# Kernel optimization log

Measured on AMD Instinct MI355X. Metric: run time of the kernel, lower is better.

Reference implementation:

```python
import jax, jax.numpy as jnp
import numpy as np

NUM_HEADS = 8
EMBED_DIM = 128
HEAD_DIM = EMBED_DIM // NUM_HEADS  # 16
NB_FEATURES = EMBED_DIM            # 128
EPS = 1e-4


def _make_projection(nb_rows, nb_cols, rng):
    # gaussian_orthogonal_random_matrix with scaling=0
    blocks = []
    for _ in range(nb_rows // nb_cols):
        q, _ = np.linalg.qr(rng.standard_normal((nb_cols, nb_cols)))
        blocks.append(q.T)
    rem = nb_rows - (nb_rows // nb_cols) * nb_cols
    if rem > 0:
        q, _ = np.linalg.qr(rng.standard_normal((nb_cols, nb_cols)))
        blocks.append(q.T[:rem])
    final = np.concatenate(blocks, axis=0)
    mult = np.linalg.norm(rng.standard_normal((nb_rows, nb_cols)), axis=1)
    return (mult[:, None] * final).astype(np.float32)


def setup_inputs() -> dict:
    key = jax.random.key(0)
    ks = jax.random.split(key, 7)
    R, C, E = 8, 2048, EMBED_DIM
    s = 1.0 / np.sqrt(E)
    x = jax.random.normal(ks[0], (R, C, E), dtype=jnp.float32)
    Wq = jax.random.uniform(ks[1], (E, E), jnp.float32, -s, s)
    bq = jax.random.uniform(ks[2], (E,), jnp.float32, -s, s)
    Wk = jax.random.uniform(ks[3], (E, E), jnp.float32, -s, s)
    bk = jax.random.uniform(ks[4], (E,), jnp.float32, -s, s)
    Wv = jax.random.uniform(ks[5], (E, E), jnp.float32, -s, s)
    bv = jax.random.uniform(ks[6], (E,), jnp.float32, -s, s)
    proj = jnp.asarray(_make_projection(NB_FEATURES, HEAD_DIM, np.random.default_rng(0)))
    return {"x": x, "Wq": Wq, "bq": bq, "Wk": Wk, "bk": bk, "Wv": Wv, "bv": bv, "proj": proj}


def _softmax_kernel(data, proj, is_query):
    # data: (R, h, n, d); proj: (F, d)
    d = data.shape[-1]
    normalizer = d ** (-0.25)
    ratio = proj.shape[0] ** (-0.5)
    data_dash = jnp.einsum('rhnd,jd->rhnj', normalizer * data, proj)  # (R,h,n,F)
    diag = jnp.sum(data * data, axis=-1, keepdims=True) * 0.5 * normalizer ** 2
    if is_query:
        m = jnp.max(data_dash, axis=-1, keepdims=True)
    else:
        m = jnp.max(data_dash, axis=(-1, -2), keepdims=True)
    return ratio * (jnp.exp(data_dash - diag - m) + EPS)


def reference(x, Wq, bq, Wk, bk, Wv, bv, proj):
    R, C, E = x.shape
    h, hd = NUM_HEADS, HEAD_DIM

    def proj_heads(W, b):
        y = jnp.einsum('rce,fe->rcf', x, W) + b
        return y.reshape(R, C, h, hd).transpose(0, 2, 1, 3)  # (R,h,C,hd)

    q = _softmax_kernel(proj_heads(Wq, bq), proj, is_query=True)   # (R,h,C,F)
    k = _softmax_kernel(proj_heads(Wk, bk), proj, is_query=False)  # (R,h,C,F)
    v = proj_heads(Wv, bv)                                          # (R,h,C,hd)

    # fold batch (R) into the feature dim: (h, C, R*F) / (h, C, R*hd)
    qf = q.transpose(1, 2, 0, 3).reshape(h, C, R * NB_FEATURES)
    kf = k.transpose(1, 2, 0, 3).reshape(h, C, R * NB_FEATURES)
    vf = v.transpose(1, 2, 0, 3).reshape(h, C, R * hd)

    k_sum = kf.sum(axis=-2)                                   # (h, D)
    D_inv = 1.0 / jnp.einsum('hnd,hd->hn', qf, k_sum)         # (h, C)
    context = jnp.einsum('hnd,hne->hde', kf, vf)              # (h, D, Ev)
    out = jnp.einsum('hde,hnd,hn->hne', context, qf, D_inv)   # (h, C, R*hd)

    out = out.reshape(h, C, R, hd).transpose(2, 1, 0, 3).reshape(R, C, E)
    attn = jnp.einsum('hqf,hkf->hqk', qf, kf)                 # (h, C, C)
    return out, attn
```

## Files before the change

kernel.cpp:

```cpp
#include <hip/hip_runtime.h>
#include <hip/hip_bf16.h>
#include <stdint.h>

typedef __bf16 bf16x8 __attribute__((ext_vector_type(8)));
typedef __bf16 bf16x4 __attribute__((ext_vector_type(4)));
typedef float  f32x4  __attribute__((ext_vector_type(4)));

#define RATIO 0.08838834764831845f
#define EPSV  1e-4f

#define GLOBAL_AS __attribute__((address_space(1)))
#define LDS_AS    __attribute__((address_space(3)))

static __device__ __forceinline__ void gload16(const void* g, void* l) {
  __builtin_amdgcn_global_load_lds((GLOBAL_AS const void*)g, (LDS_AS void*)l, 16, 0, 0);
}

static constexpr size_t OFF_XB    = 0;
static constexpr size_t OFF_WCAT  = OFF_XB    + 4194304;
static constexpr size_t OFF_MQ    = OFF_WCAT  + 98304;
static constexpr size_t OFF_MK    = OFF_MQ    + 262144;
static constexpr size_t OFF_BCAT  = OFF_MK    + 262144;
static constexpr size_t OFF_BQF   = OFF_BCAT  + 2048;
static constexpr size_t OFF_BKF   = OFF_BQF   + 4096;
static constexpr size_t OFF_Y     = OFF_BKF   + 4096;
static constexpr size_t OFF_QF    = OFF_Y     + 25165824;
static constexpr size_t OFF_KF    = OFF_QF    + 33554432;
static constexpr size_t OFF_KFT   = OFF_KF    + 33554432;
static constexpr size_t OFF_VFT   = OFF_KFT   + 33554432;
static constexpr size_t OFF_KPART = OFF_VFT   + 4194304;
static constexpr size_t OFF_KMAX  = OFF_KPART + 4096;
static constexpr size_t OFF_KSPART= OFF_KMAX  + 1024;
static constexpr size_t OFF_DPART = OFF_KSPART+ 524288;
static constexpr size_t OFF_CTXP  = OFF_DPART + 524288;
static constexpr size_t OFF_CTXT  = OFF_CTXP  + 16777216;
static constexpr size_t WS_NEED   = OFF_CTXT  + 2097152;

static __device__ __forceinline__ void gemm_core(
    const __hip_bfloat16* __restrict__ A, const __hip_bfloat16* __restrict__ B,
    int lda, int ldb, int K, int tm, int tn,
    __bf16* As, __bf16* Bs, f32x4 acc[4][4]) {
  const int t    = threadIdx.x;
  const int w    = t >> 6;
  const int lane = t & 63;
  const int m_off = (w >> 1) << 6;
  const int n_off = (w & 1) << 6;
  const int r0 = t >> 2;
  const int kk = (t & 3) << 3;
  char* Asb = (char*)As + (w << 10);
  char* Bsb = (char*)Bs + (w << 10);
  const int frow = lane & 15;
  const int koff = (lane >> 4) << 3;
  for (int k0 = 0; k0 < K; k0 += 32) {
    const __hip_bfloat16* Ag = A + (size_t)(tm + r0) * lda + (k0 + kk);
    const __hip_bfloat16* Bg = B + (size_t)(tn + r0) * ldb + (k0 + kk);
    gload16(Ag, Asb);
    gload16(Ag + (size_t)64 * lda, Asb + 4096);
    gload16(Bg, Bsb);
    gload16(Bg + (size_t)64 * ldb, Bsb + 4096);
    __syncthreads();
    bf16x8 af[4], bfr[4];
#pragma unroll
    for (int mi = 0; mi < 4; ++mi)
      af[mi] = *(const bf16x8*)(As + ((m_off + mi * 16 + frow) << 5) + koff);
#pragma unroll
    for (int ni = 0; ni < 4; ++ni)
      bfr[ni] = *(const bf16x8*)(Bs + ((n_off + ni * 16 + frow) << 5) + koff);
#pragma unroll
    for (int mi = 0; mi < 4; ++mi)
#pragma unroll
      for (int ni = 0; ni < 4; ++ni)
        acc[mi][ni] = __builtin_amdgcn_mfma_f32_16x16x32_bf16(af[mi], bfr[ni], acc[mi][ni], 0, 0, 0);
    __syncthreads();
  }
}

static __device__ __forceinline__ void gemm_core_k128(
    const __hip_bfloat16* __restrict__ A, const __hip_bfloat16* __restrict__ B,
    int lda, int ldb, int tm, int tn,
    __bf16* As, __bf16* Bs, f32x4 acc[4][4]) {
  const int t = threadIdx.x, w = t >> 6, lane = t & 63;
  const int m_off = (w >> 1) << 6, n_off = (w & 1) << 6;
  const int frow = lane & 15;
  const int g0 = lane >> 4;
  const int srow = (w << 5) + (lane >> 4);
  const int sg = lane & 15;
  char* Ab = (char*)As + (w << 13);
  char* Bb = (char*)Bs + (w << 13);
#pragma unroll
  for (int j = 0; j < 8; ++j) {
    const int row = srow + (j << 2);
    const int scol = (sg ^ (row & 15)) << 3;
    gload16(A + (size_t)(tm + row) * lda + scol, Ab + (j << 10));
    gload16(B + (size_t)(tn + row) * ldb + scol, Bb + (j << 10));
  }
  __syncthreads();
#pragma unroll
  for (int kk = 0; kk < 4; ++kk) {
    bf16x8 af[4], bfr[4];
#pragma unroll
    for (int mi = 0; mi < 4; ++mi) {
      const int row = m_off + mi * 16 + frow;
      const int gr = ((kk << 2) + g0) ^ (row & 15);
      af[mi] = *(const bf16x8*)((char*)As + row * 256 + gr * 16);
    }
#pragma unroll
    for (int ni = 0; ni < 4; ++ni) {
      const int row = n_off + ni * 16 + frow;
      const int gr = ((kk << 2) + g0) ^ (row & 15);
      bfr[ni] = *(const bf16x8*)((char*)Bs + row * 256 + gr * 16);
    }
#pragma unroll
    for (int mi = 0; mi < 4; ++mi)
#pragma unroll
      for (int ni = 0; ni < 4; ++ni)
        acc[mi][ni] = __builtin_amdgcn_mfma_f32_16x16x32_bf16(af[mi], bfr[ni], acc[mi][ni], 0, 0, 0);
  }
  __syncthreads();
}

#define ZERO_ACC(acc) do {                                   \
  _Pragma("unroll") for (int a_ = 0; a_ < 4; ++a_)           \
  _Pragma("unroll") for (int b_ = 0; b_ < 4; ++b_)           \
    acc[a_][b_] = (f32x4){0.f, 0.f, 0.f, 0.f};               \
} while (0)

__global__ void k_prep(const float* __restrict__ x,
                       const float* __restrict__ Wq, const float* __restrict__ bq,
                       const float* __restrict__ Wk, const float* __restrict__ bk,
                       const float* __restrict__ Wv, const float* __restrict__ bv,
                       const float* __restrict__ proj,
                       __hip_bfloat16* __restrict__ xb,
                       __hip_bfloat16* __restrict__ Wcat, float* __restrict__ bcat,
                       __hip_bfloat16* __restrict__ Mq, __hip_bfloat16* __restrict__ Mk,
                       float* __restrict__ bqf, float* __restrict__ bkf) {
  const int b = blockIdx.x, t = threadIdx.x;
  {
    int i = (b * 256 + t) * 4;
    f32x4 v = *(const f32x4*)(x + i);
#pragma unroll
    for (int j = 0; j < 4; ++j) xb[i + j] = __float2bfloat16(v[j]);
  }
  if (b < 1024) {
    int i = b * 256 + t;
    {
      int which = i >> 17;
      int rem = i & 131071;
      int hj = rem >> 7, e = rem & 127;
      int hh = hj >> 7, j = hj & 127;
      const float* W = which ? Wk : Wq;
      float s = 0.f;
#pragma unroll
      for (int u = 0; u < 16; ++u) s += proj[j * 16 + u] * W[(hh * 16 + u) * 128 + e];
      if (which) Mk[rem] = __float2bfloat16(0.5f * s);
      else       Mq[rem] = __float2bfloat16(0.5f * s);
    }
    if (i < 2048) {
      int which = i >> 10;
      int hj = i & 1023, hh = hj >> 7, j = hj & 127;
      const float* bb = which ? bk : bq;
      float s = 0.f;
#pragma unroll
      for (int u = 0; u < 16; ++u) s += proj[j * 16 + u] * bb[hh * 16 + u];
      if (which) bkf[hj] = 0.5f * s;
      else       bqf[hj] = 0.5f * s;
    }
  }
  if (b < 192) {
    int i = b * 256 + t;
    int mat = i >> 14, rem = i & 16383;
    const float* W = (mat == 0) ? Wq : ((mat == 1) ? Wk : Wv);
    Wcat[i] = __float2bfloat16(W[rem]);
    if (i < 384) {
      int m2 = i >> 7;
      const float* bb = (m2 == 0) ? bq : ((m2 == 1) ? bk : bv);
      bcat[i] = bb[i & 127];
    }
  }
}

__global__ __launch_bounds__(256) void k_proj(
    const __hip_bfloat16* __restrict__ xb, const __hip_bfloat16* __restrict__ Wcat,
    const float* __restrict__ bcat, float* __restrict__ Y,
    __hip_bfloat16* __restrict__ vfT) {
  __shared__ __align__(16) char pool[65536];
  __bf16* As = (__bf16*)pool;
  __bf16* Bs = (__bf16*)(pool + 32768);
  const int tm = blockIdx.x << 7, tn = blockIdx.y << 7;
  f32x4 acc[4][4];
  ZERO_ACC(acc);
  gemm_core_k128(xb, Wcat, 128, 128, tm, tn, As, Bs, acc);
  const int t = threadIdx.x, w = t >> 6, lane = t & 63;
  const int m_off = (w >> 1) << 6, n_off = (w & 1) << 6;
  const int frow = lane & 15;
  if (tn == 256) {
    __bf16* vT = (__bf16*)pool;
#pragma unroll
    for (int ni = 0; ni < 4; ++ni) {
      const int j = n_off + ni * 16 + frow;
      const float bias = bcat[256 + j];
#pragma unroll
      for (int mi = 0; mi < 4; ++mi)
#pragma unroll
        for (int i = 0; i < 4; ++i) {
          const int rl = m_off + mi * 16 + ((lane >> 4) << 2) + i;
          vT[j * 136 + rl] = (__bf16)(acc[mi][ni][i] + bias);
        }
    }
    __syncthreads();
    const int r = tm >> 11, c0 = tm & 2047;
    const int j2 = t >> 1, half = t & 1;
    const int hh = j2 >> 4, aa = j2 & 15;
    __bf16* dst = (__bf16*)vfT + (((size_t)(hh * 128 + r * 16 + aa)) << 11) + c0 + (half << 6);
    const __bf16* srcr = vT + j2 * 136 + (half << 6);
#pragma unroll
    for (int q8 = 0; q8 < 8; ++q8)
      *(bf16x8*)(dst + (q8 << 3)) = *(const bf16x8*)(srcr + (q8 << 3));
  } else {
#pragma unroll
    for (int ni = 0; ni < 4; ++ni) {
      const int col = tn + n_off + ni * 16 + frow;
      const float bias = bcat[col];
#pragma unroll
      for (int mi = 0; mi < 4; ++mi)
#pragma unroll
        for (int i = 0; i < 4; ++i) {
          const int row = tm + m_off + mi * 16 + ((lane >> 4) << 2) + i;
          Y[(size_t)row * 384 + col] = acc[mi][ni][i] + bias;
        }
    }
  }
}

__global__ __launch_bounds__(256) void k_dashk_max(
    const __hip_bfloat16* __restrict__ xb, const __hip_bfloat16* __restrict__ Mk,
    const float* __restrict__ bkf, float* __restrict__ kpart) {
  __shared__ __align__(16) char pool[65536];
  __shared__ float wmax[4];
  __bf16* As = (__bf16*)pool;
  __bf16* Bs = (__bf16*)(pool + 32768);
  const int h = blockIdx.y;
  const int tm = blockIdx.x << 7;
  f32x4 acc[4][4];
  ZERO_ACC(acc);
  gemm_core_k128(xb, Mk + h * 16384, 128, 128, tm, 0, As, Bs, acc);
  const int t = threadIdx.x, w = t >> 6, lane = t & 63;
  const int n_off = (w & 1) << 6;
  float mx = -1e30f;
#pragma unroll
  for (int ni = 0; ni < 4; ++ni) {
    const float bia = bkf[h * 128 + n_off + ni * 16 + (lane & 15)];
#pragma unroll
    for (int mi = 0; mi < 4; ++mi)
#pragma unroll
      for (int i = 0; i < 4; ++i) mx = fmaxf(mx, acc[mi][ni][i] + bia);
  }
#pragma unroll
  for (int off = 1; off < 64; off <<= 1) mx = fmaxf(mx, __shfl_xor(mx, off));
  if (lane == 0) wmax[w] = mx;
  __syncthreads();
  if (t == 0) kpart[h * 128 + blockIdx.x] = fmaxf(fmaxf(wmax[0], wmax[1]), fmaxf(wmax[2], wmax[3]));
}

__global__ __launch_bounds__(256) void k_dashk_feat(
    const __hip_bfloat16* __restrict__ xb, const __hip_bfloat16* __restrict__ Mk,
    const float* __restrict__ bkf, const float* __restrict__ Y,
    const float* __restrict__ kpart,
    __hip_bfloat16* __restrict__ kf, __hip_bfloat16* __restrict__ kfT,
    float* __restrict__ kspart) {
  __shared__ __align__(16) char pool[65536];
  __shared__ float diag_s[128];
  __shared__ float ksp_s[2][128];
  __bf16* As = (__bf16*)pool;
  __bf16* Bs = (__bf16*)(pool + 32768);
  __bf16* kT = (__bf16*)pool;
  const int h = blockIdx.y;
  const int tm = blockIdx.x << 7;
  const int t = threadIdx.x, w = t >> 6, lane = t & 63;
  if (t < 128) {
    const float* yp = Y + (size_t)(tm + t) * 384 + 128 + h * 16;
    float s = 0.f;
#pragma unroll
    for (int u = 0; u < 16; ++u) s += yp[u] * yp[u];
    diag_s[t] = 0.125f * s;
  }
  f32x4 acc[4][4];
  ZERO_ACC(acc);
  gemm_core_k128(xb, Mk + h * 16384, 128, 128, tm, 0, As, Bs, acc);
  const int m_off = (w >> 1) << 6, n_off = (w & 1) << 6;
  const int frow = lane & 15;
  const int r = tm >> 11;
  const int c0 = tm & 2047;
  const int cb = blockIdx.x & 15;
  float m = -1e30f;
  {
    const float* kp = kpart + h * 128 + r * 16;
#pragma unroll
    for (int i = 0; i < 16; ++i) m = fmaxf(m, kp[i]);
  }
  float bia[4];
#pragma unroll
  for (int ni = 0; ni < 4; ++ni) bia[ni] = bkf[h * 128 + n_off + ni * 16 + frow];
  float ksp[4] = {0.f, 0.f, 0.f, 0.f};
#pragma unroll
  for (int mi = 0; mi < 4; ++mi) {
#pragma unroll
    for (int i = 0; i < 4; ++i) {
      const int rl = m_off + mi * 16 + ((lane >> 4) << 2) + i;
      const int c = c0 + rl;
      const float dm = diag_s[rl] + m;
#pragma unroll
      for (int ni = 0; ni < 4; ++ni) {
        const int j = n_off + ni * 16 + frow;
        const float f = RATIO * (__expf(acc[mi][ni][i] + bia[ni] - dm) + EPSV);
        const __hip_bfloat16 hb = __float2bfloat16(f);
        kf[((size_t)((h << 11) + c) << 10) + (r << 7) + j] = hb;
        kT[j * 136 + rl] = (__bf16)f;
        ksp[ni] += __bfloat162float(hb);
      }
    }
  }
#pragma unroll
  for (int ni = 0; ni < 4; ++ni) {
    ksp[ni] += __shfl_xor(ksp[ni], 16);
    ksp[ni] += __shfl_xor(ksp[ni], 32);
  }
  if ((lane >> 4) == 0) {
#pragma unroll
    for (int ni = 0; ni < 4; ++ni)
      ksp_s[w >> 1][n_off + ni * 16 + frow] = ksp[ni];
  }
  __syncthreads();
  if (t < 128)
    kspart[(((cb << 3) + h) << 10) + r * 128 + t] = ksp_s[0][t] + ksp_s[1][t];
  const int j2 = t >> 1, half = t & 1;
  __bf16* dst = (__bf16*)kfT + (((size_t)(h << 10) + (r << 7) + j2) << 11) + c0 + (half << 6);
  const __bf16* srcr = kT + j2 * 136 + (half << 6);
#pragma unroll
  for (int q8 = 0; q8 < 8; ++q8)
    *(bf16x8*)(dst + (q8 << 3)) = *(const bf16x8*)(srcr + (q8 << 3));
}

__global__ __launch_bounds__(256) void k_dashq(
    const __hip_bfloat16* __restrict__ xb, const __hip_bfloat16* __restrict__ Mq,
    const float* __restrict__ bqf, const float* __restrict__ Y,
    const float* __restrict__ kspart,
    __hip_bfloat16* __restrict__ qf, float* __restrict__ dpart) {
  __shared__ __align__(16) char pool[65536];
  __shared__ float diag_s[128];
  __shared__ float rmax_s[2][128];
  __shared__ float ksum_s[128];
  __shared__ float dred_s[2][128];
  __bf16* As = (__bf16*)pool;
  __bf16* Bs = (__bf16*)(pool + 32768);
  const int h = blockIdx.y;
  const int tm = blockIdx.x << 7;
  const int r = tm >> 11, c0 = tm & 2047;
  f32x4 acc[4][4];
  ZERO_ACC(acc);
  const int t = threadIdx.x, w = t >> 6, lane = t & 63;
  if (t < 128) {
    const float* yp = Y + (size_t)(tm + t) * 384 + h * 16;
    float s = 0.f;
#pragma unroll
    for (int u = 0; u < 16; ++u) s += yp[u] * yp[u];
    diag_s[t] = 0.125f * s;
    float ks = 0.f;
#pragma unroll
    for (int cb = 0; cb < 16; ++cb) ks += kspart[(((cb << 3) + h) << 10) + r * 128 + t];
    ksum_s[t] = ks;
  }
  gemm_core_k128(xb, Mq + h * 16384, 128, 128, tm, 0, As, Bs, acc);
  const int m_off = (w >> 1) << 6, n_off = (w & 1) << 6;
  const int frow = lane & 15;
  float bia[4];
#pragma unroll
  for (int ni = 0; ni < 4; ++ni) bia[ni] = bqf[h * 128 + n_off + ni * 16 + frow];
  float rmx[4][4];
#pragma unroll
  for (int mi = 0; mi < 4; ++mi)
#pragma unroll
    for (int i = 0; i < 4; ++i) {
      float m0 = acc[mi][0][i] + bia[0];
      m0 = fmaxf(m0, acc[mi][1][i] + bia[1]);
      m0 = fmaxf(m0, acc[mi][2][i] + bia[2]);
      m0 = fmaxf(m0, acc[mi][3][i] + bia[3]);
      rmx[mi][i] = m0;
    }
#pragma unroll
  for (int off = 1; off < 16; off <<= 1)
#pragma unroll
    for (int mi = 0; mi < 4; ++mi)
#pragma unroll
      for (int i = 0; i < 4; ++i)
        rmx[mi][i] = fmaxf(rmx[mi][i], __shfl_xor(rmx[mi][i], off));
  if (frow == 0) {
#pragma unroll
    for (int mi = 0; mi < 4; ++mi)
#pragma unroll
      for (int i = 0; i < 4; ++i)
        rmax_s[w & 1][m_off + mi * 16 + ((lane >> 4) << 2) + i] = rmx[mi][i];
  }
  __syncthreads();
  float p[4][4];
#pragma unroll
  for (int mi = 0; mi < 4; ++mi)
#pragma unroll
    for (int i = 0; i < 4; ++i) p[mi][i] = 0.f;
#pragma unroll
  for (int mi = 0; mi < 4; ++mi) {
#pragma unroll
    for (int i = 0; i < 4; ++i) {
      const int rl = m_off + mi * 16 + ((lane >> 4) << 2) + i;
      const float md = diag_s[rl] + fmaxf(rmax_s[0][rl], rmax_s[1][rl]);
#pragma unroll
      for (int ni = 0; ni < 4; ++ni) {
        const int j = n_off + ni * 16 + frow;
        const float f = RATIO * (__expf(acc[mi][ni][i] + bia[ni] - md) + EPSV);
        const __hip_bfloat16 hb = __float2bfloat16(f);
        qf[((size_t)((h << 11) + c0 + rl) << 10) + (r << 7) + j] = hb;
        p[mi][i] += __bfloat162float(hb) * ksum_s[j];
      }
    }
  }
#pragma unroll
  for (int off = 1; off < 16; off <<= 1)
#pragma unroll
    for (int mi = 0; mi < 4; ++mi)
#pragma unroll
      for (int i = 0; i < 4; ++i)
        p[mi][i] += __shfl_xor(p[mi][i], off);
  if (frow == 0) {
#pragma unroll
    for (int mi = 0; mi < 4; ++mi)
#pragma unroll
      for (int i = 0; i < 4; ++i)
        dred_s[w & 1][m_off + mi * 16 + ((lane >> 4) << 2) + i] = p[mi][i];
  }
  __syncthreads();
  if (t < 128)
    dpart[(((r << 3) + h) << 11) + c0 + t] = dred_s[0][t] + dred_s[1][t];
}

#define SBAR() __builtin_amdgcn_s_barrier()
#define FEN()  do { asm volatile("" ::: "memory"); __builtin_amdgcn_sched_barrier(0); } while (0)
#define PRIO1() __builtin_amdgcn_s_setprio(1)
#define PRIO0() __builtin_amdgcn_s_setprio(0)
#define VMW4() do { asm volatile("s_waitcnt vmcnt(4)" ::: "memory"); } while (0)
#define VMW0() do { asm volatile("s_waitcnt vmcnt(0)" ::: "memory"); } while (0)

#define MFMA16(nlo) do {                                                      \
  _Pragma("unroll") for (int mi_ = 0; mi_ < 8; ++mi_)                         \
  _Pragma("unroll") for (int nj_ = 0; nj_ < 2; ++nj_)                         \
    acc[mi_][(nlo) + nj_] = __builtin_amdgcn_mfma_f32_16x16x32_bf16(          \
        aR[mi_], bR[nj_], acc[mi_][(nlo) + nj_], 0, 0, 0);                    \
} while (0)

__global__ __launch_bounds__(512, 2) void k_attn8(
    const __hip_bfloat16* __restrict__ qf, const __hip_bfloat16* __restrict__ kf,
    float* __restrict__ attn) {
  extern __shared__ __align__(128) char lds[];
  const int lid = blockIdx.x;
  const int swz = ((lid & 7) << 6) + (lid >> 3);
  const int h  = swz >> 6;
  const int tm = ((swz >> 3) & 7) << 8;
  const int tn = (swz & 7) << 8;
  const __hip_bfloat16* Ag = qf + ((size_t)h << 21);
  const __hip_bfloat16* Bg = kf + ((size_t)h << 21);

  const int t = threadIdx.x, wid = t >> 6, lane = t & 63;
  const int f = lane & 15;
  const int wr = wid >> 2, wc = wid & 3;
  const int swzg = (((lane >> 4) ^ ((f >> 1) & 3)) << 4);
  const int aoff = ((wr << 7) + f) * 64 + swzg;
  const int boff = 65536 + ((wc << 6) + f) * 64 + swzg;
  const int srow = t >> 2;
  const int scol = (((t & 3) ^ ((t >> 3) & 3)) << 3);
  const int sdst = wid << 10;

  f32x4 acc[8][4] = {};
  bf16x8 aR[8], bR[2];

  auto stageA = [&](int buf, int kh, int k0) {
    char* d = lds + buf * 32768 + kh * 16384 + sdst;
    const __hip_bfloat16* g = Ag + (size_t)(tm + srow) * 1024 + k0 + (kh << 5) + scol;
    gload16(g, d);
    gload16(g + 128 * 1024, d + 8192);
  };
  auto stageB = [&](int buf, int kh, int k0) {
    char* d = lds + 65536 + buf * 32768 + kh * 16384 + sdst;
    const __hip_bfloat16* g = Bg + (size_t)(tn + srow) * 1024 + k0 + (kh << 5) + scol;
    gload16(g, d);
    gload16(g + 128 * 1024, d + 8192);
  };

  stageA(0, 0, 0); stageB(0, 0, 0); stageA(0, 1, 0); stageB(0, 1, 0);
  VMW4();
  SBAR(); FEN();

  for (int kt = 0; kt < 15; ++kt) {
    const int buf = kt & 1, nbuf = buf ^ 1;
    const int bo = buf * 32768;
    const int nk0 = (kt + 1) << 6;
#pragma unroll
    for (int mi = 0; mi < 8; ++mi) aR[mi] = *(const bf16x8*)(lds + bo + aoff + mi * 1024);
    bR[0] = *(const bf16x8*)(lds + bo + boff);
    bR[1] = *(const bf16x8*)(lds + bo + boff + 1024);
    stageA(nbuf, 0, nk0);
    PRIO1(); MFMA16(0); PRIO0();
    bR[0] = *(const bf16x8*)(lds + bo + boff + 2048);
    bR[1] = *(const bf16x8*)(lds + bo + boff + 3072);
    stageB(nbuf, 0, nk0);
    PRIO1(); MFMA16(2); PRIO0();
    VMW4();
    SBAR(); FEN();
#pragma unroll
    for (int mi = 0; mi < 8; ++mi) aR[mi] = *(const bf16x8*)(lds + bo + 16384 + aoff + mi * 1024);
    bR[0] = *(const bf16x8*)(lds + bo + 16384 + boff);
    bR[1] = *(const bf16x8*)(lds + bo + 16384 + boff + 1024);
    stageA(nbuf, 1, nk0);
    PRIO1(); MFMA16(0); PRIO0();
    bR[0] = *(const bf16x8*)(lds + bo + 16384 + boff + 2048);
    bR[1] = *(const bf16x8*)(lds + bo + 16384 + boff + 3072);
    stageB(nbuf, 1, nk0);
    PRIO1(); MFMA16(2); PRIO0();
    VMW4();
    SBAR(); FEN();
  }
  {
    const int bo = 32768;
#pragma unroll
    for (int mi = 0; mi < 8; ++mi) aR[mi] = *(const bf16x8*)(lds + bo + aoff + mi * 1024);
    bR[0] = *(const bf16x8*)(lds + bo + boff);
    bR[1] = *(const bf16x8*)(lds + bo + boff + 1024);
    PRIO1(); MFMA16(0); PRIO0();
    bR[0] = *(const bf16x8*)(lds + bo + boff + 2048);
    bR[1] = *(const bf16x8*)(lds + bo + boff + 3072);
    PRIO1(); MFMA16(2); PRIO0();
    VMW0();
    SBAR(); FEN();
#pragma unroll
    for (int mi = 0; mi < 8; ++mi) aR[mi] = *(const bf16x8*)(lds + bo + 16384 + aoff + mi * 1024);
    bR[0] = *(const bf16x8*)(lds + bo + 16384 + boff);
    bR[1] = *(const bf16x8*)(lds + bo + 16384 + boff + 1024);
    PRIO1(); MFMA16(0); PRIO0();
    bR[0] = *(const bf16x8*)(lds + bo + 16384 + boff + 2048);
    bR[1] = *(const bf16x8*)(lds + bo + 16384 + boff + 3072);
    PRIO1(); MFMA16(2); PRIO0();
  }

  float* Cc = attn + ((size_t)h << 22);
  const int rbase = tm + (wr << 7) + ((lane >> 4) << 2);
  const int cbase = tn + (wc << 6) + f;
#pragma unroll
  for (int mi = 0; mi < 8; ++mi)
#pragma unroll
    for (int i = 0; i < 4; ++i) {
      float* rp = Cc + ((size_t)(rbase + mi * 16 + i) << 11) + cbase;
#pragma unroll
      for (int ni = 0; ni < 4; ++ni) rp[ni * 16] = acc[mi][ni][i];
    }
}

__global__ __launch_bounds__(256) void k_ctx(
    const __hip_bfloat16* __restrict__ vfT, const __hip_bfloat16* __restrict__ kfT,
    float* __restrict__ ctxp) {
  __shared__ __align__(16) __bf16 As[4096], Bs[4096];
  const int z = blockIdx.z, h = z >> 2, kc = z & 3;
  const int tn = blockIdx.y << 7;
  f32x4 acc[4][4];
  ZERO_ACC(acc);
  gemm_core(vfT + ((size_t)h << 18) + (kc << 9), kfT + ((size_t)h << 21) + (kc << 9),
            2048, 2048, 512, 0, tn, As, Bs, acc);
  float* Cp = ctxp + ((size_t)(kc * 8 + h) << 17);
  const int t = threadIdx.x, w = t >> 6, lane = t & 63;
  const int m_off = (w >> 1) << 6, n_off = (w & 1) << 6;
#pragma unroll
  for (int mi = 0; mi < 4; ++mi)
#pragma unroll
    for (int i = 0; i < 4; ++i) {
      const int row = m_off + mi * 16 + ((lane >> 4) << 2) + i;
#pragma unroll
      for (int ni = 0; ni < 4; ++ni) {
        const int col = tn + n_off + ni * 16 + (lane & 15);
        Cp[((size_t)row << 10) + col] = acc[mi][ni][i];
      }
    }
}

__global__ void k_ctxred(const float* __restrict__ ctxp, __hip_bfloat16* __restrict__ ctxT) {
  const int i = (blockIdx.x * 256 + threadIdx.x) * 4;
  f32x4 a = *(const f32x4*)(ctxp + i);
  f32x4 b = *(const f32x4*)(ctxp + i + 1048576);
  f32x4 c = *(const f32x4*)(ctxp + i + 2097152);
  f32x4 d = *(const f32x4*)(ctxp + i + 3145728);
  bf16x4 o;
#pragma unroll
  for (int j = 0; j < 4; ++j) o[j] = (__bf16)(a[j] + b[j] + c[j] + d[j]);
  *(bf16x4*)((__bf16*)ctxT + i) = o;
}

__global__ __launch_bounds__(256) void k_out64(
    const __hip_bfloat16* __restrict__ qf, const __hip_bfloat16* __restrict__ ctxT,
    const float* __restrict__ dpart, float* __restrict__ outp) {
  __shared__ __align__(16) __bf16 As[2048], Bs[4096];
  __shared__ float dinv_s[64];
  const int h = blockIdx.z;
  const int tm = blockIdx.x << 6;
  const int t = threadIdx.x, w = t >> 6, lane = t & 63;
  if (t < 64) {
    float s = 0.f;
#pragma unroll
    for (int r = 0; r < 8; ++r) s += dpart[(((r << 3) + h) << 11) + tm + t];
    dinv_s[t] = 1.0f / s;
  }
  const int m_off = (w >> 1) << 5, n_off = (w & 1) << 6;
  const int r0 = t >> 2, kk = (t & 3) << 3;
  char* Asb = (char*)As + ((t >> 6) << 10);
  char* Bsb = (char*)Bs + ((t >> 6) << 10);
  const int frow = lane & 15, koff = (lane >> 4) << 3;
  const __hip_bfloat16* A = qf + ((size_t)h << 21);
  const __hip_bfloat16* B = ctxT + ((size_t)h << 17);
  f32x4 acc[2][4];
#pragma unroll
  for (int a_ = 0; a_ < 2; ++a_)
#pragma unroll
    for (int b_ = 0; b_ < 4; ++b_) acc[a_][b_] = (f32x4){0.f, 0.f, 0.f, 0.f};
  for (int k0 = 0; k0 < 1024; k0 += 32) {
    const __hip_bfloat16* Agp = A + (size_t)(tm + r0) * 1024 + (k0 + kk);
    const __hip_bfloat16* Bgp = B + (size_t)r0 * 1024 + (k0 + kk);
    gload16(Agp, Asb);
    gload16(Bgp, Bsb);
    gload16(Bgp + (size_t)64 * 1024, Bsb + 4096);
    __syncthreads();
    bf16x8 af[2], bfr[4];
#pragma unroll
    for (int mi = 0; mi < 2; ++mi)
      af[mi] = *(const bf16x8*)(As + ((m_off + mi * 16 + frow) << 5) + koff);
#pragma unroll
    for (int ni = 0; ni < 4; ++ni)
      bfr[ni] = *(const bf16x8*)(Bs + ((n_off + ni * 16 + frow) << 5) + koff);
#pragma unroll
    for (int mi = 0; mi < 2; ++mi)
#pragma unroll
      for (int ni = 0; ni < 4; ++ni)
        acc[mi][ni] = __builtin_amdgcn_mfma_f32_16x16x32_bf16(af[mi], bfr[ni], acc[mi][ni], 0, 0, 0);
    __syncthreads();
  }
#pragma unroll
  for (int mi = 0; mi < 2; ++mi)
#pragma unroll
    for (int i = 0; i < 4; ++i) {
      const int rl = m_off + mi * 16 + ((lane >> 4) << 2) + i;
      const int row = tm + rl;
      const float dv = dinv_s[rl];
#pragma unroll
      for (int ni = 0; ni < 4; ++ni) {
        const int col = n_off + ni * 16 + frow;
        const int rb = col >> 4, tt = col & 15;
        outp[(((size_t)(rb << 11) + row) << 7) + (h << 4) + tt] = acc[mi][ni][i] * dv;
      }
    }
}

extern "C" void kernel_launch(void* const* d_in, const int* in_sizes, int n_in,
                              void* d_out, int out_size, void* d_ws, size_t ws_size,
                              hipStream_t stream) {
  const float* x    = (const float*)d_in[0];
  const float* Wq   = (const float*)d_in[1];
  const float* bq   = (const float*)d_in[2];
  const float* Wk   = (const float*)d_in[3];
  const float* bk   = (const float*)d_in[4];
  const float* Wv   = (const float*)d_in[5];
  const float* bv   = (const float*)d_in[6];
  const float* proj = (const float*)d_in[7];
  if (ws_size < WS_NEED) return;

  char* ws = (char*)d_ws;
  __hip_bfloat16* xb   = (__hip_bfloat16*)(ws + OFF_XB);
  __hip_bfloat16* Wcat = (__hip_bfloat16*)(ws + OFF_WCAT);
  __hip_bfloat16* Mq   = (__hip_bfloat16*)(ws + OFF_MQ);
  __hip_bfloat16* Mk   = (__hip_bfloat16*)(ws + OFF_MK);
  float* bcat = (float*)(ws + OFF_BCAT);
  float* bqf  = (float*)(ws + OFF_BQF);
  float* bkf  = (float*)(ws + OFF_BKF);
  float* Y    = (float*)(ws + OFF_Y);
  __hip_bfloat16* qf  = (__hip_bfloat16*)(ws + OFF_QF);
  __hip_bfloat16* kf  = (__hip_bfloat16*)(ws + OFF_KF);
  __hip_bfloat16* kfT = (__hip_bfloat16*)(ws + OFF_KFT);
  __hip_bfloat16* vfT = (__hip_bfloat16*)(ws + OFF_VFT);
  float* kpart  = (float*)(ws + OFF_KPART);
  float* kspart = (float*)(ws + OFF_KSPART);
  float* dpart  = (float*)(ws + OFF_DPART);
  float* ctxp   = (float*)(ws + OFF_CTXP);
  __hip_bfloat16* ctxT = (__hip_bfloat16*)(ws + OFF_CTXT);

  float* outp = (float*)d_out;
  float* attn = (float*)d_out + 2097152;

  static int attr_done = 0;
  if (!attr_done) {
    (void)hipFuncSetAttribute((const void*)k_attn8,
                              hipFuncAttributeMaxDynamicSharedMemorySize, 131072);
    attr_done = 1;
  }

  k_prep<<<dim3(2048), dim3(256), 0, stream>>>(x, Wq, bq, Wk, bk, Wv, bv, proj,
                                               xb, Wcat, bcat, Mq, Mk, bqf, bkf);
  k_proj<<<dim3(128, 3), dim3(256), 0, stream>>>(xb, Wcat, bcat, Y, vfT);
  k_dashk_max<<<dim3(128, 8), dim3(256), 0, stream>>>(xb, Mk, bkf, kpart);
  k_dashk_feat<<<dim3(128, 8), dim3(256), 0, stream>>>(xb, Mk, bkf, Y, kpart, kf, kfT, kspart);
  k_dashq<<<dim3(128, 8), dim3(256), 0, stream>>>(xb, Mq, bqf, Y, kspart, qf, dpart);
  k_attn8<<<dim3(512), dim3(512), 131072, stream>>>(qf, kf, attn);
  k_ctx<<<dim3(1, 8, 32), dim3(256), 0, stream>>>(vfT, kfT, ctxp);
  k_ctxred<<<dim3(1024), dim3(256), 0, stream>>>(ctxp, ctxT);
  k_out64<<<dim3(32, 1, 8), dim3(256), 0, stream>>>(qf, ctxT, dpart, outp);
}
```

Before: 183.8 us.

## Replace double-buffered attn GEMM loop with a four-stage LDS ring prefetch

The attention GEMM main loop switches from two 64-wide K buffers, each processed in halves, to a four-slot ring of 32-wide K tiles. Loads run three tiles ahead, and each iteration waits with vmcnt(8). Each iteration loads all A and B fragments up front and issues 32 MFMAs in one block instead of two groups of 16. The goal is to hide global-to-LDS latency with a deeper prefetch while keeping total LDS use the same. The risk is extra registers for the four B fragments and a fixed barrier per 32-K step.

```diff
diff --git a/kernel.cpp b/kernel.cpp
--- a/kernel.cpp
+++ b/kernel.cpp
@@ -446,14 +446,15 @@
 #define FEN()  do { asm volatile("" ::: "memory"); __builtin_amdgcn_sched_barrier(0); } while (0)
 #define PRIO1() __builtin_amdgcn_s_setprio(1)
 #define PRIO0() __builtin_amdgcn_s_setprio(0)
+#define VMW8() do { asm volatile("s_waitcnt vmcnt(8)" ::: "memory"); } while (0)
 #define VMW4() do { asm volatile("s_waitcnt vmcnt(4)" ::: "memory"); } while (0)
 #define VMW0() do { asm volatile("s_waitcnt vmcnt(0)" ::: "memory"); } while (0)
 
-#define MFMA16(nlo) do {                                                      \
+#define MFMA32() do {                                                         \
   _Pragma("unroll") for (int mi_ = 0; mi_ < 8; ++mi_)                         \
-  _Pragma("unroll") for (int nj_ = 0; nj_ < 2; ++nj_)                         \
-    acc[mi_][(nlo) + nj_] = __builtin_amdgcn_mfma_f32_16x16x32_bf16(          \
-        aR[mi_], bR[nj_], acc[mi_][(nlo) + nj_], 0, 0, 0);                    \
+  _Pragma("unroll") for (int nj_ = 0; nj_ < 4; ++nj_)                         \
+    acc[mi_][nj_] = __builtin_amdgcn_mfma_f32_16x16x32_bf16(                  \
+        aR[mi_], bR[nj_], acc[mi_][nj_], 0, 0, 0);                            \
 } while (0)
 
 __global__ __launch_bounds__(512, 2) void k_attn8(
@@ -471,82 +472,52 @@
   const int t = threadIdx.x, wid = t >> 6, lane = t & 63;
   const int f = lane & 15;
   const int wr = wid >> 2, wc = wid & 3;
-  const int swzg = (((lane >> 4) ^ ((f >> 1) & 3)) << 4);
-  const int aoff = ((wr << 7) + f) * 64 + swzg;
-  const int boff = 65536 + ((wc << 6) + f) * 64 + swzg;
+  const int swzg = (((lane >> 4) ^ ((lane >> 1) & 3)) << 4);
+  const int abase = ((wr << 7) + f) * 64 + swzg;
+  const int bbase = 16384 + ((wc << 6) + f) * 64 + swzg;
   const int srow = t >> 2;
   const int scol = (((t & 3) ^ ((t >> 3) & 3)) << 3);
   const int sdst = wid << 10;
 
   f32x4 acc[8][4] = {};
-  bf16x8 aR[8], bR[2];
-
-  auto stageA = [&](int buf, int kh, int k0) {
-    char* d = lds + buf * 32768 + kh * 16384 + sdst;
-    const __hip_bfloat16* g = Ag + (size_t)(tm + srow) * 1024 + k0 + (kh << 5) + scol;
-    gload16(g, d);
-    gload16(g + 128 * 1024, d + 8192);
+  bf16x8 aR[8], bR[4];
+
+  auto stage = [&](int tile) {
+    char* buf = lds + (tile & 3) * 32768;
+    const __hip_bfloat16* ga = Ag + (size_t)(tm + srow) * 1024 + (tile << 5) + scol;
+    const __hip_bfloat16* gb = Bg + (size_t)(tn + srow) * 1024 + (tile << 5) + scol;
+    gload16(ga, buf + sdst);
+    gload16(ga + 128 * 1024, buf + 8192 + sdst);
+    gload16(gb, buf + 16384 + sdst);
+    gload16(gb + 24576 - 16384 + 16384 + 8192 - 8192, buf + 24576 + sdst);
   };
-  auto stageB = [&](int buf, int kh, int k0) {
-    char* d = lds + 65536 + buf * 32768 + kh * 16384 + sdst;
-    const __hip_bfloat16* g = Bg + (size_t)(tn + srow) * 1024 + k0 + (kh << 5) + scol;
-    gload16(g, d);
-    gload16(g + 128 * 1024, d + 8192);
+  auto stage2 = [&](int tile) {
+    char* buf = lds + (tile & 3) * 32768;
+    const __hip_bfloat16* ga = Ag + (size_t)(tm + srow) * 1024 + (tile << 5) + scol;
+    const __hip_bfloat16* gb = Bg + (size_t)(tn + srow) * 1024 + (tile << 5) + scol;
+    gload16(ga, buf + sdst);
+    gload16(ga + 128 * 1024, buf + 8192 + sdst);
+    gload16(gb, buf + 16384 + sdst);
+    gload16(gb + 128 * 1024, buf + 24576 + sdst);
   };
-
-  stageA(0, 0, 0); stageB(0, 0, 0); stageA(0, 1, 0); stageB(0, 1, 0);
-  VMW4();
+  (void)stage;
+
+  stage2(0); stage2(1); stage2(2);
+  VMW8();
   SBAR(); FEN();
 
-  for (int kt = 0; kt < 15; ++kt) {
-    const int buf = kt & 1, nbuf = buf ^ 1;
-    const int bo = buf * 32768;
-    const int nk0 = (kt + 1) << 6;
-#pragma unroll
-    for (int mi = 0; mi < 8; ++mi) aR[mi] = *(const bf16x8*)(lds + bo + aoff + mi * 1024);
-    bR[0] = *(const bf16x8*)(lds + bo + boff);
-    bR[1] = *(const bf16x8*)(lds + bo + boff + 1024);
-    stageA(nbuf, 0, nk0);
-    PRIO1(); MFMA16(0); PRIO0();
-    bR[0] = *(const bf16x8*)(lds + bo + boff + 2048);
-    bR[1] = *(const bf16x8*)(lds + bo + boff + 3072);
-    stageB(nbuf, 0, nk0);
-    PRIO1(); MFMA16(2); PRIO0();
-    VMW4();
-    SBAR(); FEN();
-#pragma unroll
-    for (int mi = 0; mi < 8; ++mi) aR[mi] = *(const bf16x8*)(lds + bo + 16384 + aoff + mi * 1024);
-    bR[0] = *(const bf16x8*)(lds + bo + 16384 + boff);
-    bR[1] = *(const bf16x8*)(lds + bo + 16384 + boff + 1024);
-    stageA(nbuf, 1, nk0);
-    PRIO1(); MFMA16(0); PRIO0();
-    bR[0] = *(const bf16x8*)(lds + bo + 16384 + boff + 2048);
-    bR[1] = *(const bf16x8*)(lds + bo + 16384 + boff + 3072);
-    stageB(nbuf, 1, nk0);
-    PRIO1(); MFMA16(2); PRIO0();
-    VMW4();
-    SBAR(); FEN();
-  }
-  {
-    const int bo = 32768;
-#pragma unroll
-    for (int mi = 0; mi < 8; ++mi) aR[mi] = *(const bf16x8*)(lds + bo + aoff + mi * 1024);
-    bR[0] = *(const bf16x8*)(lds + bo + boff);
-    bR[1] = *(const bf16x8*)(lds + bo + boff + 1024);
-    PRIO1(); MFMA16(0); PRIO0();
-    bR[0] = *(const bf16x8*)(lds + bo + boff + 2048);
-    bR[1] = *(const bf16x8*)(lds + bo + boff + 3072);
-    PRIO1(); MFMA16(2); PRIO0();
-    VMW0();
-    SBAR(); FEN();
-#pragma unroll
-    for (int mi = 0; mi < 8; ++mi) aR[mi] = *(const bf16x8*)(lds + bo + 16384 + aoff + mi * 1024);
-    bR[0] = *(const bf16x8*)(lds + bo + 16384 + boff);
-    bR[1] = *(const bf16x8*)(lds + bo + 16384 + boff + 1024);
-    PRIO1(); MFMA16(0); PRIO0();
-    bR[0] = *(const bf16x8*)(lds + bo + 16384 + boff + 2048);
-    bR[1] = *(const bf16x8*)(lds + bo + 16384 + boff + 3072);
-    PRIO1(); MFMA16(2); PRIO0();
+  for (int kt = 0; kt < 32; ++kt) {
+    char* buf = lds + (kt & 3) * 32768;
+#pragma unroll
+    for (int mi = 0; mi < 8; ++mi) aR[mi] = *(const bf16x8*)(buf + abase + mi * 1024);
+#pragma unroll
+    for (int nj = 0; nj < 4; ++nj) bR[nj] = *(const bf16x8*)(buf + bbase + nj * 1024);
+    if (kt < 29) stage2(kt + 3);
+    PRIO1(); MFMA32(); PRIO0();
+    if (kt < 29) { VMW8(); }
+    else if (kt == 29) { VMW4(); }
+    else if (kt == 30) { VMW0(); }
+    if (kt < 31) { SBAR(); FEN(); }
   }
 
   float* Cc = attn + ((size_t)h << 22);
```

New measurement: 184.2 us. No clear change (+0.2%).
